# Kernel optimization log

Hardware: AMD Instinct MI355X
Metric: run time of the kernel (lower is better)

Reference implementation:

```python
import jax, jax.numpy as jnp
import numpy as np

B, L, CH, NH, NB = 32, 512, 512, 8, 2
HD = CH // NH
NEG = -4294967295.0  # -2**32 + 1, as in the torch code


def _ln(x, g, b, eps=1e-8):
    m = x.mean(-1, keepdims=True)
    v = ((x - m) ** 2).mean(-1, keepdims=True)
    return (x - m) / jnp.sqrt(v + eps) * g + b


def _forward(log_seqs, seqs_nxt, t, qw, qb, kw, kb, vw, vb,
             ln1g, ln1b, ln2g, ln2b, c1w, c1b, c2w, c2b,
             posK, posV, lng, lnb, tw0, tb0, tw1, tb1, tw2, tb2,
             decw, decb):
    # causal mask (mode='training'): True = masked (~tril)
    mask = jnp.triu(jnp.ones((L, L), dtype=bool), k=1)
    pK = posK[:L].reshape(L, NH, HD)  # shared relative/absolute pos per head
    pV = posV[:L].reshape(L, NH, HD)
    seqs = log_seqs
    for i in range(NB):
        Qin = _ln(seqs, ln1g[i], ln1b[i])
        # note: Q from layernormed input, K/V from raw seqs (as in torch code)
        Q = (Qin @ qw[i].T + qb[i]).reshape(B, L, NH, HD)
        K = (seqs @ kw[i].T + kb[i]).reshape(B, L, NH, HD)
        V = (seqs @ vw[i].T + vb[i]).reshape(B, L, NH, HD)
        scores = jnp.einsum('blhd,bmhd->bhlm', Q, K)
        scores = scores + jnp.einsum('blhd,mhd->bhlm', Q, pK)
        scores = scores / jnp.sqrt(jnp.float32(HD))
        scores = jnp.where(mask, NEG, scores)
        w = jax.nn.softmax(scores, axis=-1)
        out = jnp.einsum('bhlm,bmhd->blhd', w, V) + jnp.einsum('bhlm,mhd->blhd', w, pV)
        seqs = Qin + out.reshape(B, L, CH)  # residual from layernormed Q
        seqs = _ln(seqs, ln2g[i], ln2b[i])
        # PointWiseFeedForward: conv1d kernel_size=1 == linear; residual inside
        h = jax.nn.relu(seqs @ c1w[i].T + c1b[i])
        seqs = seqs + (h @ c2w[i].T + c2b[i])
    log_feats = _ln(seqs, lng, lnb)

    # diffusion timestep embedding
    half = CH // 2
    freqs = jnp.exp(jnp.arange(half, dtype=jnp.float32) * (-np.log(10000.0) / (half - 1)))
    ang = t.astype(jnp.float32)[:, None] * freqs[None, :]
    temb = jnp.concatenate([jnp.sin(ang), jnp.cos(ang)], axis=1)  # [B, CH]
    temb = temb @ tw0.T + tb0
    temb = temb * jax.nn.sigmoid(temb)  # swish nonlinearity
    temb = temb @ tw1.T + tb1
    temb = temb * jax.nn.sigmoid(temb)
    temb = temb @ tw2.T + tb2
    x_t = seqs_nxt + temb[:, None, :]

    # non-conditional decoder path: decoder(cat([log_feats, x_t], -1))
    dec = jnp.concatenate([log_feats, x_t], axis=-1) @ decw.T + decb
    return (log_feats, dec)


def setup_inputs() -> dict:
    key = jax.random.key(0)
    ks = jax.random.split(key, 24)
    s = 0.02

    def n(k, shape):
        return jax.random.normal(k, shape, jnp.float32) * s

    return {
        'log_seqs': jax.random.normal(ks[0], (B, L, CH), jnp.float32),
        'seqs_nxt': jax.random.normal(ks[1], (B, L, CH), jnp.float32),
        't': jax.random.randint(ks[2], (B,), 0, 1000, jnp.int32),
        'qw': n(ks[3], (NB, CH, CH)), 'qb': jnp.zeros((NB, CH), jnp.float32),
        'kw': n(ks[4], (NB, CH, CH)), 'kb': jnp.zeros((NB, CH), jnp.float32),
        'vw': n(ks[5], (NB, CH, CH)), 'vb': jnp.zeros((NB, CH), jnp.float32),
        'ln1g': jnp.ones((NB, CH), jnp.float32), 'ln1b': jnp.zeros((NB, CH), jnp.float32),
        'ln2g': jnp.ones((NB, CH), jnp.float32), 'ln2b': jnp.zeros((NB, CH), jnp.float32),
        'c1w': n(ks[6], (NB, CH, CH)), 'c1b': jnp.zeros((NB, CH), jnp.float32),
        'c2w': n(ks[7], (NB, CH, CH)), 'c2b': jnp.zeros((NB, CH), jnp.float32),
        'posK': n(ks[8], (L, CH)), 'posV': n(ks[9], (L, CH)),
        'lng': jnp.ones((CH,), jnp.float32), 'lnb': jnp.zeros((CH,), jnp.float32),
        'tw0': n(ks[10], (4 * CH, CH)), 'tb0': jnp.zeros((4 * CH,), jnp.float32),
        'tw1': n(ks[11], (4 * CH, 4 * CH)), 'tb1': jnp.zeros((4 * CH,), jnp.float32),
        'tw2': n(ks[12], (CH, 4 * CH)), 'tb2': jnp.zeros((CH,), jnp.float32),
        'decw': n(ks[13], (CH, 2 * CH)), 'decb': jnp.zeros((CH,), jnp.float32),
    }


def reference(log_seqs, seqs_nxt, t, qw, qb, kw, kb, vw, vb,
              ln1g, ln1b, ln2g, ln2b, c1w, c1b, c2w, c2b,
              posK, posV, lng, lnb, tw0, tb0, tw1, tb1, tw2, tb2,
              decw, decb):
    return _forward(log_seqs, seqs_nxt, t, qw, qb, kw, kb, vw, vb,
                    ln1g, ln1b, ln2g, ln2b, c1w, c1b, c2w, c2b,
                    posK, posV, lng, lnb, tw0, tb0, tw1, tb1, tw2, tb2,
                    decw, decb)
```

## Files before the change

### kernel.cpp

```cpp
#include <hip/hip_runtime.h>
#include <math.h>

#define BB 32
#define LL 512
#define CHN 512
#define NHH 8
#define HDD 64

typedef __attribute__((ext_vector_type(8))) short short8;
typedef __attribute__((ext_vector_type(4))) float f32x4;

__device__ __forceinline__ float b2f(unsigned short s) {
    union { unsigned int u; float f; } c; c.u = ((unsigned int)s) << 16; return c.f;
}
__device__ __forceinline__ unsigned short f2b(float f) {
    union { float f; unsigned int u; } c; c.f = f;
    return (unsigned short)((c.u + 0x7fffu + ((c.u >> 16) & 1u)) >> 16);
}

#define SWZ(row, col) ((((row) * 64 + (col))) ^ (((row) & 7) << 3))

__device__ __forceinline__ void gl16(const unsigned short* g, unsigned short* l) {
    __builtin_amdgcn_global_load_lds(
        (const __attribute__((address_space(1))) unsigned int*)g,
        (__attribute__((address_space(3))) unsigned int*)l, 16, 0, 0);
}

__global__ __launch_bounds__(256) void cvt7_kernel(
    const float* __restrict__ p0, const float* __restrict__ p1,
    const float* __restrict__ p2, const float* __restrict__ p3,
    const float* __restrict__ p4, const float* __restrict__ p5,
    unsigned short* __restrict__ y,
    const float* __restrict__ seqs, unsigned short* __restrict__ R1)
{
    const int j = blockIdx.y;
    const int i = blockIdx.x * 256 + threadIdx.x;
    if (j < 6) {
        const float* x = j == 0 ? p0 : j == 1 ? p1 : j == 2 ? p2
                       : j == 3 ? p3 : j == 4 ? p4 : p5;
        const float4 v = reinterpret_cast<const float4*>(x)[i];
        ushort4 o;
        o.x = f2b(v.x); o.y = f2b(v.y); o.z = f2b(v.z); o.w = f2b(v.w);
        size_t dst4;
        if (j == 1)      dst4 = 131072 + i + (i >= 65536 ? 65536 : 0);
        else if (j == 2) dst4 = 131072 + 65536 + i + (i >= 65536 ? 65536 : 0);
        else             dst4 = (size_t)j * 131072 + i;
        reinterpret_cast<ushort4*>(y)[dst4] = o;
    } else {
        #pragma unroll
        for (int t = 0; t < 16; ++t) {
            const int ii = t * 131072 + i;
            const float4 v = reinterpret_cast<const float4*>(seqs)[ii];
            ushort4 o;
            o.x = f2b(v.x); o.y = f2b(v.y); o.z = f2b(v.z); o.w = f2b(v.w);
            reinterpret_cast<ushort4*>(R1)[ii] = o;
        }
    }
}

__global__ __launch_bounds__(256) void ln_kernel(
    const unsigned short* __restrict__ x, const float* __restrict__ g,
    const float* __restrict__ b, float* __restrict__ yf,
    unsigned short* __restrict__ yb)
{
    const int row = blockIdx.x;
    const int tid = threadIdx.x;
    const size_t base = (size_t)row * CHN;
    const ushort2 v2 = *reinterpret_cast<const ushort2*>(x + base + tid * 2);
    const float vx = b2f(v2.x), vy = b2f(v2.y);
    float s  = vx + vy;
    float ss = vx * vx + vy * vy;
    #pragma unroll
    for (int m = 1; m < 64; m <<= 1) {
        s  += __shfl_xor(s, m);
        ss += __shfl_xor(ss, m);
    }
    __shared__ float red[8];
    const int wave = tid >> 6;
    if ((tid & 63) == 0) { red[wave] = s; red[4 + wave] = ss; }
    __syncthreads();
    s  = red[0] + red[1] + red[2] + red[3];
    ss = red[4] + red[5] + red[6] + red[7];
    const float mean = s * (1.0f / CHN);
    const float var  = ss * (1.0f / CHN) - mean * mean;
    const float inv  = rsqrtf(var + 1e-8f);
    const int c = tid * 2;
    float ox = (vx - mean) * inv * g[c]     + b[c];
    float oy = (vy - mean) * inv * g[c + 1] + b[c + 1];
    if (yf) *reinterpret_cast<float2*>(yf + base + c) = make_float2(ox, oy);
    if (yb) {
        ushort2 ob; ob.x = f2b(ox); ob.y = f2b(oy);
        *reinterpret_cast<ushort2*>(yb + base + c) = ob;
    }
}

template <int NT, int NBX>
__device__ __forceinline__ void gemm_body(
    const unsigned short* __restrict__ A,
    const unsigned short* __restrict__ A2,
    const unsigned short* __restrict__ W, int ldw,
    const float* __restrict__ bias,
    const float* __restrict__ pos,
    const unsigned short* __restrict__ resb,
    float* __restrict__ outf,
    unsigned short* __restrict__ outb,
    unsigned short* __restrict__ outbt,
    int act, int bid,
    unsigned short* lA, unsigned short* lB)
{
    const int tid  = threadIdx.x;
    const int lane = tid & 63;
    const int wid  = tid >> 6;

    const int swz = (bid & 7) * (NBX * 8) + (bid >> 3);
    const int by = swz / NBX, bx = swz % NBX;
    const int bm = by * 256, bn = bx * 128;

    const int ia0 = wid * 2, ia1 = wid * 2 + 1;
    const int hiA0 = ia0 >> 2, rgA0 = ia0 & 3;
    const int hiA1 = ia1 >> 2, rgA1 = ia1 & 3;
    const int hiB = wid >> 1, rgB = wid & 1;

    const unsigned short* Ax = A2 ? A2 : A;
    const unsigned short* aS0  = A  + (size_t)(bm + rgA0 * 64 + lane) * 512 + hiA0 * 8;
    const unsigned short* aS1  = A  + (size_t)(bm + rgA1 * 64 + lane) * 512 + hiA1 * 8;
    const unsigned short* a2S0 = Ax + (size_t)(bm + rgA0 * 64 + lane) * 512 + hiA0 * 8;
    const unsigned short* a2S1 = Ax + (size_t)(bm + rgA1 * 64 + lane) * 512 + hiA1 * 8;
    const unsigned short* wS   = W + (size_t)(bn + rgB * 64 + lane) * ldw + hiB * 8;
    const int dA0 = (hiA0 * 256 + rgA0 * 64) * 8;
    const int dA1 = (hiA1 * 256 + rgA1 * 64) * 8;
    const int dB  = (hiB * 128 + rgB * 64) * 8;

    const int wr = wid >> 1, wc = wid & 1;
    const int fr = lane & 15;
    const int fq = lane >> 4;

    f32x4 acc[4][4];
    #pragma unroll
    for (int m = 0; m < 4; ++m)
        #pragma unroll
        for (int n = 0; n < 4; ++n)
            acc[m][n] = (f32x4){0.f, 0.f, 0.f, 0.f};

    #define MG_STAGE(buf, t)                                            \
        do {                                                            \
            const int k0 = ((t) & 15) * 32;                             \
            const unsigned short* s0 = ((t) < 16) ? aS0 : a2S0;         \
            const unsigned short* s1 = ((t) < 16) ? aS1 : a2S1;         \
            gl16(s0 + k0, &lA[(buf) * 8192 + dA0]);                     \
            gl16(s1 + k0, &lA[(buf) * 8192 + dA1]);                     \
            gl16(wS + (t) * 32, &lB[(buf) * 4096 + dB]);                \
        } while (0)

    MG_STAGE(0, 0);
    MG_STAGE(1, 1);

    #pragma unroll
    for (int t = 0; t < NT; ++t) {
        const int cur = t % 3;
        if (t + 2 < NT) {
            MG_STAGE((t + 2) % 3, t + 2);
            asm volatile("s_waitcnt vmcnt(6)" ::: "memory");
        } else if (t + 1 < NT) {
            asm volatile("s_waitcnt vmcnt(3)" ::: "memory");
        } else {
            asm volatile("s_waitcnt vmcnt(0)" ::: "memory");
        }
        __builtin_amdgcn_s_barrier();

        const unsigned short* pa = &lA[cur * 8192 + (fq * 256 + wr * 64 + fr) * 8];
        const unsigned short* pb = &lB[cur * 4096 + (fq * 128 + wc * 64 + fr) * 8];
        short8 aF[4], bF[4];
        #pragma unroll
        for (int m = 0; m < 4; ++m)
            aF[m] = *reinterpret_cast<const short8*>(pa + m * 128);
        #pragma unroll
        for (int n = 0; n < 4; ++n)
            bF[n] = *reinterpret_cast<const short8*>(pb + n * 128);
        asm volatile("s_waitcnt lgkmcnt(0)" ::: "memory");
        __builtin_amdgcn_s_barrier();

        __builtin_amdgcn_s_setprio(1);
        #pragma unroll
        for (int m = 0; m < 4; ++m)
            #pragma unroll
            for (int n = 0; n < 4; ++n)
                acc[m][n] = __builtin_amdgcn_mfma_f32_16x16x32_bf16(
                    aF[m], bF[n], acc[m][n], 0, 0, 0);
        __builtin_amdgcn_s_setprio(0);
    }
    #undef MG_STAGE

    const int row0 = bm + wr * 64, col0 = bn + wc * 64;
    #pragma unroll
    for (int m = 0; m < 4; ++m) {
        #pragma unroll
        for (int n = 0; n < 4; ++n) {
            const int col = col0 + n * 16 + fr;
            const float bia = bias ? bias[col] : 0.f;
            ushort4 o4;
            #pragma unroll
            for (int r = 0; r < 4; ++r) {
                const int row = row0 + m * 16 + fq * 4 + r;
                float v = acc[m][n][r] + bia;
                if (pos) v += pos[(size_t)(row & (LL - 1)) * CHN + col];
                if (act == 1) v = fmaxf(v, 0.f);
                else if (act == 3) v *= 0.125f;
                const size_t idx = (size_t)row * CHN + col;
                if (resb) v += b2f(resb[idx]);
                if (outf) outf[idx] = v;
                if (outb) outb[idx] = f2b(v);
                ((unsigned short*)&o4)[r] = f2b(v);
            }
            if (outbt) {
                const int rw = row0 + m * 16 + fq * 4;
                *reinterpret_cast<ushort4*>(
                    &outbt[((size_t)(rw >> 9) * 512 + col) * 512 + (rw & 511)]) = o4;
            }
        }
    }
}

__device__ __forceinline__ void kv_body(
    const unsigned short* __restrict__ A,
    const unsigned short* __restrict__ Wkv,
    const float* __restrict__ kb, const float* __restrict__ vb,
    const float* __restrict__ posK, const float* __restrict__ posV,
    unsigned short* __restrict__ KBb, unsigned short* __restrict__ VTb,
    int bid, unsigned short* lA, unsigned short* lB)
{
    const int tid  = threadIdx.x;
    const int lane = tid & 63;
    const int wid  = tid >> 6;

    const int swz = (bid & 7) * 64 + (bid >> 3);
    const int by = swz >> 3, bx = swz & 7;
    const int bm = by * 256, bn = bx * 128;

    const int ia0 = wid * 2, ia1 = wid * 2 + 1;
    const int hiA0 = ia0 >> 2, rgA0 = ia0 & 3;
    const int hiA1 = ia1 >> 2, rgA1 = ia1 & 3;
    const int hiB = wid >> 1, rgB = wid & 1;

    const unsigned short* aS0 = A + (size_t)(bm + rgA0 * 64 + lane) * 512 + hiA0 * 8;
    const unsigned short* aS1 = A + (size_t)(bm + rgA1 * 64 + lane) * 512 + hiA1 * 8;
    const unsigned short* wS  = Wkv + (size_t)(bn + rgB * 64 + lane) * 512 + hiB * 8;
    const int dA0 = (hiA0 * 256 + rgA0 * 64) * 8;
    const int dA1 = (hiA1 * 256 + rgA1 * 64) * 8;
    const int dB  = (hiB * 128 + rgB * 64) * 8;

    const int wr = wid >> 1, wc = wid & 1;
    const int fr = lane & 15;
    const int fq = lane >> 4;

    f32x4 acc[4][4];
    #pragma unroll
    for (int m = 0; m < 4; ++m)
        #pragma unroll
        for (int n = 0; n < 4; ++n)
            acc[m][n] = (f32x4){0.f, 0.f, 0.f, 0.f};

    #define KV_STAGE(buf, t)                                            \
        do {                                                            \
            const int k0 = (t) * 32;                                    \
            gl16(aS0 + k0, &lA[(buf) * 8192 + dA0]);                    \
            gl16(aS1 + k0, &lA[(buf) * 8192 + dA1]);                    \
            gl16(wS + k0, &lB[(buf) * 4096 + dB]);                      \
        } while (0)

    KV_STAGE(0, 0);
    KV_STAGE(1, 1);

    #pragma unroll
    for (int t = 0; t < 16; ++t) {
        const int cur = t % 3;
        if (t + 2 < 16) {
            KV_STAGE((t + 2) % 3, t + 2);
            asm volatile("s_waitcnt vmcnt(6)" ::: "memory");
        } else if (t + 1 < 16) {
            asm volatile("s_waitcnt vmcnt(3)" ::: "memory");
        } else {
            asm volatile("s_waitcnt vmcnt(0)" ::: "memory");
        }
        __builtin_amdgcn_s_barrier();

        const unsigned short* pa = &lA[cur * 8192 + (fq * 256 + wr * 64 + fr) * 8];
        const unsigned short* pb = &lB[cur * 4096 + (fq * 128 + wc * 64 + fr) * 8];
        short8 aF[4], bF[4];
        #pragma unroll
        for (int m = 0; m < 4; ++m)
            aF[m] = *reinterpret_cast<const short8*>(pa + m * 128);
        #pragma unroll
        for (int n = 0; n < 4; ++n)
            bF[n] = *reinterpret_cast<const short8*>(pb + n * 128);
        asm volatile("s_waitcnt lgkmcnt(0)" ::: "memory");
        __builtin_amdgcn_s_barrier();

        __builtin_amdgcn_s_setprio(1);
        #pragma unroll
        for (int m = 0; m < 4; ++m)
            #pragma unroll
            for (int n = 0; n < 4; ++n)
                acc[m][n] = __builtin_amdgcn_mfma_f32_16x16x32_bf16(
                    aF[m], bF[n], acc[m][n], 0, 0, 0);
        __builtin_amdgcn_s_setprio(0);
    }
    #undef KV_STAGE

    const int row0 = bm + wr * 64;
    if (bn < 512) {
        const int col0 = bn + wc * 64;
        #pragma unroll
        for (int m = 0; m < 4; ++m) {
            #pragma unroll
            for (int n = 0; n < 4; ++n) {
                const int col = col0 + n * 16 + fr;
                const float bia = kb[col];
                #pragma unroll
                for (int r = 0; r < 4; ++r) {
                    const int row = row0 + m * 16 + fq * 4 + r;
                    float v = acc[m][n][r] + bia
                            + posK[(size_t)(row & (LL - 1)) * CHN + col];
                    KBb[(size_t)row * CHN + col] = f2b(v);
                }
            }
        }
    } else {
        const int vcol0 = (bn - 512) + wc * 64;
        #pragma unroll
        for (int m = 0; m < 4; ++m) {
            #pragma unroll
            for (int n = 0; n < 4; ++n) {
                const int vcol = vcol0 + n * 16 + fr;
                const float bia = vb[vcol];
                ushort4 o4;
                #pragma unroll
                for (int r = 0; r < 4; ++r) {
                    const int row = row0 + m * 16 + fq * 4 + r;
                    float v = acc[m][n][r] + bia
                            + posV[(size_t)(row & (LL - 1)) * CHN + vcol];
                    ((unsigned short*)&o4)[r] = f2b(v);
                }
                const int rw = row0 + m * 16 + fq * 4;
                *reinterpret_cast<ushort4*>(
                    &VTb[((size_t)(rw >> 9) * 512 + vcol) * 512 + (rw & 511)]) = o4;
            }
        }
    }
}

__global__ __launch_bounds__(512) void mgemm_kernel(
    const unsigned short* __restrict__ A,
    const unsigned short* __restrict__ W, int ldw,
    const float* __restrict__ bias,
    const float* __restrict__ pos,
    const unsigned short* __restrict__ resb,
    float* __restrict__ outf,
    unsigned short* __restrict__ outb,
    unsigned short* __restrict__ outbt,
    int act)
{
    __shared__ alignas(16) unsigned short lA[3 * 8192];
    __shared__ alignas(16) unsigned short lB[3 * 4096];
    gemm_body<16, 4>(A, nullptr, W, ldw, bias, pos, resb, outf, outb, outbt, act,
                     blockIdx.x, lA, lB);
}

__global__ __launch_bounds__(512) void qkv2_kernel(
    const unsigned short* __restrict__ qinb, const unsigned short* __restrict__ curb,
    const unsigned short* __restrict__ Wq, const unsigned short* __restrict__ Wkv,
    const float* __restrict__ qb, const float* __restrict__ kb,
    const float* __restrict__ vb,
    const float* __restrict__ posK, const float* __restrict__ posV,
    unsigned short* __restrict__ QBb, unsigned short* __restrict__ KBb,
    unsigned short* __restrict__ VTb)
{
    __shared__ alignas(16) unsigned short lA[3 * 8192];
    __shared__ alignas(16) unsigned short lB[3 * 4096];
    if (blockIdx.x < 256) {
        gemm_body<16, 4>(qinb, nullptr, Wq, 512, qb, nullptr, nullptr,
                         nullptr, QBb, nullptr, 3, blockIdx.x, lA, lB);
    } else {
        kv_body(curb, Wkv, kb, vb, posK, posV, KBb, VTb, blockIdx.x - 256, lA, lB);
    }
}

__global__ __launch_bounds__(512) void dec_kernel(
    const unsigned short* __restrict__ R0b, const unsigned short* __restrict__ R1b,
    const unsigned short* __restrict__ Wd, const float* __restrict__ decb,
    float* __restrict__ dec)
{
    __shared__ alignas(16) unsigned short lA[3 * 8192];
    __shared__ alignas(16) unsigned short lB[3 * 4096];
    gemm_body<32, 4>(R0b, R1b, Wd, 1024, decb, nullptr, nullptr, dec, nullptr,
                     nullptr, 0, blockIdx.x, lA, lB);
}

__global__ __launch_bounds__(256) void skgemm_kernel(
    const float* __restrict__ A, int K,
    const float* __restrict__ W, int N,
    float* __restrict__ P)
{
    __shared__ float As[32][128];
    const int tid = threadIdx.x;
    const int kz  = blockIdx.y;
    const int c   = blockIdx.x * 256 + tid;

    #pragma unroll
    for (int i = 0; i < 16; ++i) {
        const int idx = i * 256 + tid;
        const int r = idx >> 7, k = idx & 127;
        As[r][k] = A[(size_t)r * K + kz * 128 + k];
    }
    __syncthreads();

    float acc[32];
    #pragma unroll
    for (int r = 0; r < 32; ++r) acc[r] = 0.f;

    const float* wrow = W + (size_t)c * K + kz * 128;
    for (int k4 = 0; k4 < 32; ++k4) {
        const float4 w = reinterpret_cast<const float4*>(wrow)[k4];
        #pragma unroll
        for (int r = 0; r < 32; ++r) {
            const float4 a = *reinterpret_cast<const float4*>(&As[r][k4 * 4]);
            acc[r] = fmaf(w.x, a.x, fmaf(w.y, a.y, fmaf(w.z, a.z, fmaf(w.w, a.w, acc[r]))));
        }
    }

    float* pp = P + ((size_t)kz * N + c) * 32;
    #pragma unroll
    for (int r = 0; r < 32; ++r) pp[r] = acc[r];
}

__global__ __launch_bounds__(256) void skreduce_kernel(
    const float* __restrict__ P, int KS, const float* __restrict__ bias,
    float* __restrict__ out, int N, int act)
{
    const int idx = blockIdx.x * 256 + threadIdx.x;
    const int r = idx & 31, c = idx >> 5;
    float s = 0.f;
    for (int kz = 0; kz < KS; ++kz)
        s += P[(size_t)kz * N * 32 + idx];
    s += bias[c];
    if (act == 2) s = s / (1.f + __expf(-s));
    out[(size_t)r * N + c] = s;
}

__global__ __launch_bounds__(512) void mattn_kernel(
    const unsigned short* __restrict__ Q, const unsigned short* __restrict__ K,
    const unsigned short* __restrict__ VT, const unsigned short* __restrict__ Qin,
    unsigned short* __restrict__ Sout)
{
    __shared__ alignas(16) unsigned short kT[2][4096];
    __shared__ alignas(16) unsigned short vT[2][4096];
    __shared__ unsigned short pl[8][1024];

    const int pr = blockIdx.x;
    const int qtA = pr, qtB = 7 - pr;
    const int h  = blockIdx.y;
    const int b  = blockIdx.z;
    const int tid = threadIdx.x, lane = tid & 63, wid = tid >> 6;
    const int wg = wid >> 2;
    const int wl = wid & 3;
    const int fr = lane & 15, fq = lane >> 4;
    const int hc = h * HDD;

    const int rs = tid >> 3, js = tid & 7, ds = ((js ^ (rs & 7)) << 3);
    const unsigned short* kS = K + (size_t)b * LL * CHN + (size_t)rs * CHN + hc + ds;
    const unsigned short* vS = VT + ((size_t)(b * NHH + h) * 64 + rs) * 512 + ds;

    #define AT_STAGE(buf, ch)                                              \
        do {                                                               \
            const int o = (ch) * 64;                                       \
            gl16(kS + (size_t)o * CHN, &kT[buf][wid * 512]);               \
            gl16(vS + o, &vT[buf][wid * 512]);                             \
        } while (0)

    const int myQt = wg ? qtA : qtB;
    const size_t qrow = (size_t)b * LL + myQt * 64 + wl * 16 + fr;
    short8 qf[2];
    qf[0] = *reinterpret_cast<const short8*>(Q + qrow * CHN + hc + fq * 8);
    qf[1] = *reinterpret_cast<const short8*>(Q + qrow * CHN + hc + 32 + fq * 8);

    f32x4 oacc[4];
    float lrow[4];
    #pragma unroll
    for (int n = 0; n < 4; ++n) oacc[n] = (f32x4){0.f, 0.f, 0.f, 0.f};
    #pragma unroll
    for (int r = 0; r < 4; ++r) lrow[r] = 0.f;

    AT_STAGE(0, 0);
    __syncthreads();

    for (int ch = 0; ch <= qtB; ++ch) {
        const int cur = ch & 1;
        if (ch < qtB) AT_STAGE(cur ^ 1, ch + 1);

        if (ch <= myQt) {
            f32x4 sacc[4];
            #pragma unroll
            for (int n = 0; n < 4; ++n) sacc[n] = (f32x4){0.f, 0.f, 0.f, 0.f};
            __builtin_amdgcn_s_setprio(1);
            #pragma unroll
            for (int kk = 0; kk < 2; ++kk) {
                #pragma unroll
                for (int n = 0; n < 4; ++n) {
                    const short8 kf = *reinterpret_cast<const short8*>(
                        &kT[cur][SWZ(n * 16 + fr, kk * 32 + fq * 8)]);
                    sacc[n] = __builtin_amdgcn_mfma_f32_16x16x32_bf16(
                        qf[kk], kf, sacc[n], 0, 0, 0);
                }
            }
            __builtin_amdgcn_s_setprio(0);

            const bool diag = (ch == myQt);
            #pragma unroll
            for (int r = 0; r < 4; ++r) {
                float sv[4];
                #pragma unroll
                for (int n = 0; n < 4; ++n) {
                    float v = sacc[n][r];
                    if (diag && (n * 16 + fr > wl * 16 + fq * 4 + r)) v = -1e30f;
                    sv[n] = __expf(v);
                }
                float ps = (sv[0] + sv[1]) + (sv[2] + sv[3]);
                ps += __shfl_xor(ps, 1);
                ps += __shfl_xor(ps, 2);
                ps += __shfl_xor(ps, 4);
                ps += __shfl_xor(ps, 8);
                lrow[r] += ps;
                #pragma unroll
                for (int n = 0; n < 4; ++n)
                    pl[wid][SWZ(fq * 4 + r, n * 16 + fr)] = f2b(sv[n]);
            }

            __builtin_amdgcn_s_setprio(1);
            #pragma unroll
            for (int kk = 0; kk < 2; ++kk) {
                const short8 pa = *reinterpret_cast<const short8*>(
                    &pl[wid][SWZ(fr, kk * 32 + fq * 8)]);
                #pragma unroll
                for (int n = 0; n < 4; ++n) {
                    const short8 vf = *reinterpret_cast<const short8*>(
                        &vT[cur][SWZ(n * 16 + fr, kk * 32 + fq * 8)]);
                    oacc[n] = __builtin_amdgcn_mfma_f32_16x16x32_bf16(
                        pa, vf, oacc[n], 0, 0, 0);
                }
            }
            __builtin_amdgcn_s_setprio(0);
        }

        __syncthreads();
    }
    #undef AT_STAGE

    const size_t orow0 = (size_t)b * LL + myQt * 64 + wl * 16 + fq * 4;
    #pragma unroll
    for (int r = 0; r < 4; ++r) {
        const float inv = 1.f / lrow[r];
        const size_t rowidx = (orow0 + r) * CHN + hc;
        #pragma unroll
        for (int n = 0; n < 4; ++n) {
            const int d = n * 16 + fr;
            Sout[rowidx + d] = f2b(oacc[n][r] * inv + b2f(Qin[rowidx + d]));
        }
    }
}

__global__ __launch_bounds__(256) void temb_embed_kernel(
    const int* __restrict__ t, float* __restrict__ T0)
{
    const int idx = blockIdx.x * 256 + threadIdx.x;
    const int b = idx >> 9, j = idx & 511;
    const float tv = (float)t[b];
    const int jj = (j < 256) ? j : j - 256;
    const float freq = __expf((float)jj * (-9.210340371976184f / 255.f));
    const float ang = tv * freq;
    T0[idx] = (j < 256) ? sinf(ang) : cosf(ang);
}

__global__ __launch_bounds__(256) void add_temb_kernel(
    const float* __restrict__ xin, const float* __restrict__ temb,
    unsigned short* __restrict__ out)
{
    const size_t i4 = (size_t)blockIdx.x * 256 + threadIdx.x;
    const size_t elem = i4 * 4;
    const int b = (int)(elem >> 18);
    const int c = (int)(elem & (CHN - 1));
    const float4 a = reinterpret_cast<const float4*>(xin)[i4];
    const float4 tv = *reinterpret_cast<const float4*>(temb + (size_t)b * CHN + c);
    ushort4 o;
    o.x = f2b(a.x + tv.x); o.y = f2b(a.y + tv.y);
    o.z = f2b(a.z + tv.z); o.w = f2b(a.w + tv.w);
    reinterpret_cast<ushort4*>(out)[i4] = o;
}

extern "C" void kernel_launch(void* const* d_in, const int* in_sizes, int n_in,
                              void* d_out, int out_size, void* d_ws, size_t ws_size,
                              hipStream_t stream)
{
    (void)in_sizes; (void)n_in; (void)out_size; (void)ws_size;
    const float* log_seqs = (const float*)d_in[0];
    const float* seqs_nxt = (const float*)d_in[1];
    const int*   tt       = (const int*)d_in[2];
    const float* qw  = (const float*)d_in[3];
    const float* qb  = (const float*)d_in[4];
    const float* kw  = (const float*)d_in[5];
    const float* kb  = (const float*)d_in[6];
    const float* vw  = (const float*)d_in[7];
    const float* vb  = (const float*)d_in[8];
    const float* ln1g = (const float*)d_in[9];
    const float* ln1b = (const float*)d_in[10];
    const float* ln2g = (const float*)d_in[11];
    const float* ln2b = (const float*)d_in[12];
    const float* c1w = (const float*)d_in[13];
    const float* c1b = (const float*)d_in[14];
    const float* c2w = (const float*)d_in[15];
    const float* c2b = (const float*)d_in[16];
    const float* posK = (const float*)d_in[17];
    const float* posV = (const float*)d_in[18];
    const float* lng = (const float*)d_in[19];
    const float* lnb = (const float*)d_in[20];
    const float* tw0 = (const float*)d_in[21];
    const float* tb0 = (const float*)d_in[22];
    const float* tw1 = (const float*)d_in[23];
    const float* tb1 = (const float*)d_in[24];
    const float* tw2 = (const float*)d_in[25];
    const float* tb2 = (const float*)d_in[26];
    const float* decw = (const float*)d_in[27];
    const float* decb = (const float*)d_in[28];

    const size_t SZ = (size_t)BB * LL * CHN;
    const int M = BB * LL;
    float* out = (float*)d_out;
    float* log_feats = out;
    float* dec = out + SZ;
    unsigned short* QBb = (unsigned short*)dec;
    unsigned short* VTb = (unsigned short*)log_feats;

    float* ws = (float*)d_ws;
    unsigned short* SB = (unsigned short*)ws;
    float* P = ws + SZ / 2;
    unsigned short* KBb = (unsigned short*)(ws + SZ);
    unsigned short* R0  = (unsigned short*)(ws + SZ + SZ / 2);
    unsigned short* R1  = (unsigned short*)(ws + 2 * SZ);
    unsigned short* WBu = (unsigned short*)(ws + 2 * SZ + SZ / 2);
    float* T0 = ws + 2 * SZ + SZ / 2 + 1572864;
    float* T1 = T0 + 32 * CHN;
    float* T2 = T1 + 32 * 2048;
    float* T3 = T2 + 32 * 2048;

    const size_t WQ = 0, WKV = 524288, WC1 = 1572864,
                 WC2 = 2097152, WDEC = 2621440;

    auto mg = [&](const unsigned short* A, const unsigned short* W, int ldw,
                  const float* bias, const float* pos, const unsigned short* resb,
                  float* outf, unsigned short* outb, unsigned short* outbt, int act) {
        mgemm_kernel<<<256, 512, 0, stream>>>(A, W, ldw, bias, pos, resb,
                                              outf, outb, outbt, act);
    };
    auto skg = [&](const float* A, int K, const float* W, int N,
                   const float* bias, float* o, int act) {
        skgemm_kernel<<<dim3(N / 256, K / 128), 256, 0, stream>>>(A, K, W, N, P);
        skreduce_kernel<<<(N * 32) / 256, 256, 0, stream>>>(P, K / 128, bias, o, N, act);
    };

    cvt7_kernel<<<dim3(512, 7), 256, 0, stream>>>(qw, kw, vw, c1w, c2w, decw, WBu,
                                                  log_seqs, R1);

    for (int i = 0; i < 2; ++i) {
        const size_t wo = (size_t)i * 262144;
        const size_t bo = (size_t)i * CHN;

        ln_kernel<<<M, 256, 0, stream>>>(R1, ln1g + bo, ln1b + bo, nullptr, R0);
        qkv2_kernel<<<768, 512, 0, stream>>>(
            R0, R1, WBu + WQ + wo, WBu + WKV + (size_t)i * 524288,
            qb + bo, kb + bo, vb + bo, posK, posV, QBb, KBb, VTb);
        mattn_kernel<<<dim3(4, NHH, BB), 512, 0, stream>>>(QBb, KBb, VTb, R0, SB);
        ln_kernel<<<M, 256, 0, stream>>>(SB, ln2g + bo, ln2b + bo, nullptr, SB);
        mg(SB, WBu + WC1 + wo, 512, c1b + bo, nullptr, nullptr, nullptr, R0, nullptr, 1);
        mg(R0, WBu + WC2 + wo, 512, c2b + bo, nullptr, SB, nullptr, R1, nullptr, 0);
    }

    ln_kernel<<<M, 256, 0, stream>>>(R1, lng, lnb, log_feats, R0);

    temb_embed_kernel<<<(BB * CHN) / 256, 256, 0, stream>>>(tt, T0);
    skg(T0, 512, tw0, 2048, tb0, T1, 2);
    skg(T1, 2048, tw1, 2048, tb1, T2, 2);
    skg(T2, 2048, tw2, 512, tb2, T3, 0);
    add_temb_kernel<<<(M * CHN / 4) / 256, 256, 0, stream>>>(seqs_nxt, T3, R1);

    dec_kernel<<<256, 512, 0, stream>>>(R0, R1, WBu + WDEC, decb, dec);
}
```

Measured before the change: 591.3 us.

## Piggyback timestep-embedding MLP stages onto transformer kernels as extra blocks

The separate launches for the timestep embedding, its three split-K fp32 GEMMs with their reductions, and the temb add are removed. Each stage now runs as extra blocks appended to the grids of the ln, qkv and FFN GEMM kernels, chosen through an XJob descriptor, and the sin/cos embedding moves into the initial convert kernel. This cuts the number of launches and lets the small, latency-bound temb chain overlap with the large transformer kernels. The cost is extra branching and a larger parameter struct in those kernels, and correctness depends on the stages staying ordered across launches and on the reuse of the KBb buffer as the x_t output.

Measured after the change: 582.0 us. About the same (-1.6%).

```diff
diff --git a/kernel.cpp b/kernel.cpp
--- a/kernel.cpp
+++ b/kernel.cpp
@@ -26,12 +26,79 @@
         (__attribute__((address_space(3))) unsigned int*)l, 16, 0, 0);
 }
 
-__global__ __launch_bounds__(256) void cvt7_kernel(
+struct XJob {
+    int kind;
+    const float* a;
+    const float* w;
+    float* o;
+    unsigned short* ob;
+    int K, N, nbx, KS, act;
+};
+
+__device__ __forceinline__ void run_xjob(const XJob xj, int bid, int tid,
+                                         int nthr, float* AsRaw)
+{
+    if (xj.kind == 1) {
+        float (*As)[128] = reinterpret_cast<float(*)[128]>(AsRaw);
+        const int cb = bid % xj.nbx, kz = bid / xj.nbx;
+        for (int i = tid; i < 4096; i += nthr) {
+            const int r = i >> 7, k = i & 127;
+            As[r][k] = xj.a[(size_t)r * xj.K + kz * 128 + k];
+        }
+        __syncthreads();
+        if (tid < 256) {
+            const int c = cb * 256 + tid;
+            float acc[32];
+            #pragma unroll
+            for (int r = 0; r < 32; ++r) acc[r] = 0.f;
+            const float* wrow = xj.w + (size_t)c * xj.K + kz * 128;
+            for (int k4 = 0; k4 < 32; ++k4) {
+                const float4 w4 = reinterpret_cast<const float4*>(wrow)[k4];
+                #pragma unroll
+                for (int r = 0; r < 32; ++r) {
+                    const float4 a4 = *reinterpret_cast<const float4*>(&As[r][k4 * 4]);
+                    acc[r] = fmaf(w4.x, a4.x, fmaf(w4.y, a4.y,
+                              fmaf(w4.z, a4.z, fmaf(w4.w, a4.w, acc[r]))));
+                }
+            }
+            float* pp = xj.o + ((size_t)kz * xj.N + c) * 32;
+            #pragma unroll
+            for (int r = 0; r < 32; ++r) pp[r] = acc[r];
+        }
+    } else if (xj.kind == 2) {
+        if (tid < 256) {
+            const int idx = bid * 256 + tid;
+            const int r = idx & 31, c = idx >> 5;
+            float s = 0.f;
+            for (int kz = 0; kz < xj.KS; ++kz)
+                s += xj.a[(size_t)kz * xj.N * 32 + idx];
+            s += xj.w[c];
+            if (xj.act == 2) s = s / (1.f + __expf(-s));
+            xj.o[(size_t)r * xj.N + c] = s;
+        }
+    } else if (xj.kind == 3) {
+        if (tid < 256) {
+            const size_t i4 = (size_t)bid * 256 + tid;
+            const size_t elem = i4 * 4;
+            const int b = (int)(elem >> 18);
+            const int c = (int)(elem & (CHN - 1));
+            const float4 a = reinterpret_cast<const float4*>(xj.a)[i4];
+            const float4 tv = *reinterpret_cast<const float4*>(xj.w + (size_t)b * CHN + c);
+            ushort4 o;
+            o.x = f2b(a.x + tv.x); o.y = f2b(a.y + tv.y);
+            o.z = f2b(a.z + tv.z); o.w = f2b(a.w + tv.w);
+            reinterpret_cast<ushort4*>(xj.ob)[i4] = o;
+        }
+    }
+}
+
+__global__ __launch_bounds__(256) void cvt8_kernel(
     const float* __restrict__ p0, const float* __restrict__ p1,
     const float* __restrict__ p2, const float* __restrict__ p3,
     const float* __restrict__ p4, const float* __restrict__ p5,
     unsigned short* __restrict__ y,
-    const float* __restrict__ seqs, unsigned short* __restrict__ R1)
+    const float* __restrict__ seqs, unsigned short* __restrict__ R1,
+    const int* __restrict__ tt, float* __restrict__ T0)
 {
     const int j = blockIdx.y;
     const int i = blockIdx.x * 256 + threadIdx.x;
@@ -46,7 +113,7 @@
         else if (j == 2) dst4 = 131072 + 65536 + i + (i >= 65536 ? 65536 : 0);
         else             dst4 = (size_t)j * 131072 + i;
         reinterpret_cast<ushort4*>(y)[dst4] = o;
-    } else {
+    } else if (j == 6) {
         #pragma unroll
         for (int t = 0; t < 16; ++t) {
             const int ii = t * 131072 + i;
@@ -55,14 +122,30 @@
             o.x = f2b(v.x); o.y = f2b(v.y); o.z = f2b(v.z); o.w = f2b(v.w);
             reinterpret_cast<ushort4*>(R1)[ii] = o;
         }
+    } else {
+        if (blockIdx.x < 64) {
+            const int idx = blockIdx.x * 256 + threadIdx.x;
+            const int b = idx >> 9, jj0 = idx & 511;
+            const float tv = (float)tt[b];
+            const int jj = (jj0 < 256) ? jj0 : jj0 - 256;
+            const float freq = __expf((float)jj * (-9.210340371976184f / 255.f));
+            const float ang = tv * freq;
+            T0[idx] = (jj0 < 256) ? sinf(ang) : cosf(ang);
+        }
     }
 }
 
 __global__ __launch_bounds__(256) void ln_kernel(
     const unsigned short* __restrict__ x, const float* __restrict__ g,
     const float* __restrict__ b, float* __restrict__ yf,
-    unsigned short* __restrict__ yb)
-{
+    unsigned short* __restrict__ yb, int mainBlocks, XJob xj)
+{
+    __shared__ float red[8];
+    __shared__ alignas(16) float lnAs[4096];
+    if ((int)blockIdx.x >= mainBlocks) {
+        run_xjob(xj, blockIdx.x - mainBlocks, threadIdx.x, 256, lnAs);
+        return;
+    }
     const int row = blockIdx.x;
     const int tid = threadIdx.x;
     const size_t base = (size_t)row * CHN;
@@ -75,7 +158,6 @@
         s  += __shfl_xor(s, m);
         ss += __shfl_xor(ss, m);
     }
-    __shared__ float red[8];
     const int wave = tid >> 6;
     if ((tid & 63) == 0) { red[wave] = s; red[4 + wave] = ss; }
     __syncthreads();
@@ -358,10 +440,14 @@
     float* __restrict__ outf,
     unsigned short* __restrict__ outb,
     unsigned short* __restrict__ outbt,
-    int act)
+    int act, int mainBlocks, XJob xj)
 {
     __shared__ alignas(16) unsigned short lA[3 * 8192];
     __shared__ alignas(16) unsigned short lB[3 * 4096];
+    if ((int)blockIdx.x >= mainBlocks) {
+        run_xjob(xj, blockIdx.x - mainBlocks, threadIdx.x, 512, (float*)lA);
+        return;
+    }
     gemm_body<16, 4>(A, nullptr, W, ldw, bias, pos, resb, outf, outb, outbt, act,
                      blockIdx.x, lA, lB);
 }
@@ -373,10 +459,14 @@
     const float* __restrict__ vb,
     const float* __restrict__ posK, const float* __restrict__ posV,
     unsigned short* __restrict__ QBb, unsigned short* __restrict__ KBb,
-    unsigned short* __restrict__ VTb)
+    unsigned short* __restrict__ VTb, XJob xj)
 {
     __shared__ alignas(16) unsigned short lA[3 * 8192];
     __shared__ alignas(16) unsigned short lB[3 * 4096];
+    if (blockIdx.x >= 768) {
+        run_xjob(xj, blockIdx.x - 768, threadIdx.x, 512, (float*)lA);
+        return;
+    }
     if (blockIdx.x < 256) {
         gemm_body<16, 4>(qinb, nullptr, Wq, 512, qb, nullptr, nullptr,
                          nullptr, QBb, nullptr, 3, blockIdx.x, lA, lB);
@@ -394,57 +484,6 @@
     __shared__ alignas(16) unsigned short lB[3 * 4096];
     gemm_body<32, 4>(R0b, R1b, Wd, 1024, decb, nullptr, nullptr, dec, nullptr,
                      nullptr, 0, blockIdx.x, lA, lB);
-}
-
-__global__ __launch_bounds__(256) void skgemm_kernel(
-    const float* __restrict__ A, int K,
-    const float* __restrict__ W, int N,
-    float* __restrict__ P)
-{
-    __shared__ float As[32][128];
-    const int tid = threadIdx.x;
-    const int kz  = blockIdx.y;
-    const int c   = blockIdx.x * 256 + tid;
-
-    #pragma unroll
-    for (int i = 0; i < 16; ++i) {
-        const int idx = i * 256 + tid;
-        const int r = idx >> 7, k = idx & 127;
-        As[r][k] = A[(size_t)r * K + kz * 128 + k];
-    }
-    __syncthreads();
-
-    float acc[32];
-    #pragma unroll
-    for (int r = 0; r < 32; ++r) acc[r] = 0.f;
-
-    const float* wrow = W + (size_t)c * K + kz * 128;
-    for (int k4 = 0; k4 < 32; ++k4) {
-        const float4 w = reinterpret_cast<const float4*>(wrow)[k4];
-        #pragma unroll
-        for (int r = 0; r < 32; ++r) {
-            const float4 a = *reinterpret_cast<const float4*>(&As[r][k4 * 4]);
-            acc[r] = fmaf(w.x, a.x, fmaf(w.y, a.y, fmaf(w.z, a.z, fmaf(w.w, a.w, acc[r]))));
-        }
-    }
-
-    float* pp = P + ((size_t)kz * N + c) * 32;
-    #pragma unroll
-    for (int r = 0; r < 32; ++r) pp[r] = acc[r];
-}
-
-__global__ __launch_bounds__(256) void skreduce_kernel(
-    const float* __restrict__ P, int KS, const float* __restrict__ bias,
-    float* __restrict__ out, int N, int act)
-{
-    const int idx = blockIdx.x * 256 + threadIdx.x;
-    const int r = idx & 31, c = idx >> 5;
-    float s = 0.f;
-    for (int kz = 0; kz < KS; ++kz)
-        s += P[(size_t)kz * N * 32 + idx];
-    s += bias[c];
-    if (act == 2) s = s / (1.f + __expf(-s));
-    out[(size_t)r * N + c] = s;
 }
 
 __global__ __launch_bounds__(512) void mattn_kernel(
@@ -566,34 +605,6 @@
             Sout[rowidx + d] = f2b(oacc[n][r] * inv + b2f(Qin[rowidx + d]));
         }
     }
-}
-
-__global__ __launch_bounds__(256) void temb_embed_kernel(
-    const int* __restrict__ t, float* __restrict__ T0)
-{
-    const int idx = blockIdx.x * 256 + threadIdx.x;
-    const int b = idx >> 9, j = idx & 511;
-    const float tv = (float)t[b];
-    const int jj = (j < 256) ? j : j - 256;
-    const float freq = __expf((float)jj * (-9.210340371976184f / 255.f));
-    const float ang = tv * freq;
-    T0[idx] = (j < 256) ? sinf(ang) : cosf(ang);
-}
-
-__global__ __launch_bounds__(256) void add_temb_kernel(
-    const float* __restrict__ xin, const float* __restrict__ temb,
-    unsigned short* __restrict__ out)
-{
-    const size_t i4 = (size_t)blockIdx.x * 256 + threadIdx.x;
-    const size_t elem = i4 * 4;
-    const int b = (int)(elem >> 18);
-    const int c = (int)(elem & (CHN - 1));
-    const float4 a = reinterpret_cast<const float4*>(xin)[i4];
-    const float4 tv = *reinterpret_cast<const float4*>(temb + (size_t)b * CHN + c);
-    ushort4 o;
-    o.x = f2b(a.x + tv.x); o.y = f2b(a.y + tv.y);
-    o.z = f2b(a.z + tv.z); o.w = f2b(a.w + tv.w);
-    reinterpret_cast<ushort4*>(out)[i4] = o;
 }
 
 extern "C" void kernel_launch(void* const* d_in, const int* in_sizes, int n_in,
@@ -650,46 +661,74 @@
     float* T1 = T0 + 32 * CHN;
     float* T2 = T1 + 32 * 2048;
     float* T3 = T2 + 32 * 2048;
+    unsigned short* XT = KBb;
 
     const size_t WQ = 0, WKV = 524288, WC1 = 1572864,
                  WC2 = 2097152, WDEC = 2621440;
 
-    auto mg = [&](const unsigned short* A, const unsigned short* W, int ldw,
-                  const float* bias, const float* pos, const unsigned short* resb,
-                  float* outf, unsigned short* outb, unsigned short* outbt, int act) {
-        mgemm_kernel<<<256, 512, 0, stream>>>(A, W, ldw, bias, pos, resb,
-                                              outf, outb, outbt, act);
+    XJob xnone; xnone.kind = 0;
+    xnone.a = nullptr; xnone.w = nullptr; xnone.o = nullptr; xnone.ob = nullptr;
+    xnone.K = 0; xnone.N = 0; xnone.nbx = 1; xnone.KS = 0; xnone.act = 0;
+
+    auto mkgemm = [&](const float* A, const float* W, float* Pp, int K, int N) {
+        XJob x = xnone; x.kind = 1; x.a = A; x.w = W; x.o = Pp;
+        x.K = K; x.N = N; x.nbx = N / 256;
+        return x;
     };
-    auto skg = [&](const float* A, int K, const float* W, int N,
-                   const float* bias, float* o, int act) {
-        skgemm_kernel<<<dim3(N / 256, K / 128), 256, 0, stream>>>(A, K, W, N, P);
-        skreduce_kernel<<<(N * 32) / 256, 256, 0, stream>>>(P, K / 128, bias, o, N, act);
+    auto mkred = [&](const float* Pp, const float* bias, float* o,
+                     int KS, int N, int act) {
+        XJob x = xnone; x.kind = 2; x.a = Pp; x.w = bias; x.o = o;
+        x.KS = KS; x.N = N; x.act = act;
+        return x;
     };
 
-    cvt7_kernel<<<dim3(512, 7), 256, 0, stream>>>(qw, kw, vw, c1w, c2w, decw, WBu,
-                                                  log_seqs, R1);
+    cvt8_kernel<<<dim3(512, 8), 256, 0, stream>>>(qw, kw, vw, c1w, c2w, decw, WBu,
+                                                  log_seqs, R1, tt, T0);
 
     for (int i = 0; i < 2; ++i) {
         const size_t wo = (size_t)i * 262144;
         const size_t bo = (size_t)i * CHN;
 
-        ln_kernel<<<M, 256, 0, stream>>>(R1, ln1g + bo, ln1b + bo, nullptr, R0);
-        qkv2_kernel<<<768, 512, 0, stream>>>(
+        XJob xln1 = (i == 0) ? mkgemm(T0, tw0, P, 512, 2048)
+                             : mkred(P, tb2, T3, 16, 512, 0);
+        const int xln1n = (i == 0) ? (2048 / 256) * (512 / 128) : (512 * 32) / 256;
+        ln_kernel<<<M + xln1n, 256, 0, stream>>>(R1, ln1g + bo, ln1b + bo,
+                                                 nullptr, R0, M, xln1);
+
+        XJob xqkv = (i == 0) ? mkred(P, tb0, T1, 4, 2048, 2) : xnone;
+        const int xqkvn = (i == 0) ? (2048 * 32) / 256 : 0;
+        qkv2_kernel<<<768 + xqkvn, 512, 0, stream>>>(
             R0, R1, WBu + WQ + wo, WBu + WKV + (size_t)i * 524288,
-            qb + bo, kb + bo, vb + bo, posK, posV, QBb, KBb, VTb);
+            qb + bo, kb + bo, vb + bo, posK, posV, QBb, KBb, VTb, xqkv);
+
         mattn_kernel<<<dim3(4, NHH, BB), 512, 0, stream>>>(QBb, KBb, VTb, R0, SB);
-        ln_kernel<<<M, 256, 0, stream>>>(SB, ln2g + bo, ln2b + bo, nullptr, SB);
-        mg(SB, WBu + WC1 + wo, 512, c1b + bo, nullptr, nullptr, nullptr, R0, nullptr, 1);
-        mg(R0, WBu + WC2 + wo, 512, c2b + bo, nullptr, SB, nullptr, R1, nullptr, 0);
-    }
-
-    ln_kernel<<<M, 256, 0, stream>>>(R1, lng, lnb, log_feats, R0);
-
-    temb_embed_kernel<<<(BB * CHN) / 256, 256, 0, stream>>>(tt, T0);
-    skg(T0, 512, tw0, 2048, tb0, T1, 2);
-    skg(T1, 2048, tw1, 2048, tb1, T2, 2);
-    skg(T2, 2048, tw2, 512, tb2, T3, 0);
-    add_temb_kernel<<<(M * CHN / 4) / 256, 256, 0, stream>>>(seqs_nxt, T3, R1);
-
-    dec_kernel<<<256, 512, 0, stream>>>(R0, R1, WBu + WDEC, decb, dec);
-}
+
+        XJob xln2;
+        int xln2n;
+        if (i == 0) {
+            xln2 = mkgemm(T1, tw1, P, 2048, 2048);
+            xln2n = (2048 / 256) * (2048 / 128);
+        } else {
+            xln2 = xnone; xln2.kind = 3; xln2.a = seqs_nxt; xln2.w = T3; xln2.ob = XT;
+            xln2n = (int)(SZ / 4 / 256);
+        }
+        ln_kernel<<<M + xln2n, 256, 0, stream>>>(SB, ln2g + bo, ln2b + bo,
+                                                 nullptr, SB, M, xln2);
+
+        XJob xc1 = (i == 0) ? mkred(P, tb1, T2, 16, 2048, 2) : xnone;
+        const int xc1n = (i == 0) ? (2048 * 32) / 256 : 0;
+        mgemm_kernel<<<256 + xc1n, 512, 0, stream>>>(
+            SB, WBu + WC1 + wo, 512, c1b + bo, nullptr, nullptr,
+            nullptr, R0, nullptr, 1, 256, xc1);
+
+        XJob xc2 = (i == 0) ? mkgemm(T2, tw2, P, 2048, 512) : xnone;
+        const int xc2n = (i == 0) ? (512 / 256) * (2048 / 128) : 0;
+        mgemm_kernel<<<256 + xc2n, 512, 0, stream>>>(
+            R0, WBu + WC2 + wo, 512, c2b + bo, nullptr, SB,
+            nullptr, R1, nullptr, 0, 256, xc2);
+    }
+
+    ln_kernel<<<M, 256, 0, stream>>>(R1, lng, lnb, log_feats, R0, M, xnone);
+
+    dec_kernel<<<256, 512, 0, stream>>>(R0, XT, WBu + WDEC, decb, dec);
+}
```
